# Kernel tuning notes

Hardware: AMD Instinct MI355X
Metric: run time of the kernel (lower is better)

The kernel has to match this reference:

```python
import jax, jax.numpy as jnp
import numpy as np

N = 6144      # total atoms
F = 128       # hidden_dim
NB = 48       # number of molecules (batch segments)
LONG_RANGE_SCALE = 1.0


def setup_inputs() -> dict:
    key = jax.random.key(0)
    ks = jax.random.split(key, 16)
    s = 1.0 / np.sqrt(F)
    return {
        "h0": jax.random.normal(ks[0], (N, F), jnp.float32),
        "h1": jax.random.normal(ks[1], (N, 3, F), jnp.float32),
        "pos": jax.random.normal(ks[2], (N, 3), jnp.float32),
        "batch": jnp.sort(jax.random.randint(ks[3], (N,), 0, NB)),
        "qW1": jax.random.normal(ks[4], (F, F // 2), jnp.float32) * s,
        "qb1": jnp.zeros((F // 2,), jnp.float32),
        "qW2": jax.random.normal(ks[5], (F // 2, 1), jnp.float32) * s,
        "qb2": jnp.zeros((1,), jnp.float32),
        "cW1": jax.random.normal(ks[6], (F, F // 2), jnp.float32) * s,
        "cb1": jnp.zeros((F // 2,), jnp.float32),
        "cW2": jax.random.normal(ks[7], (F // 2, 1), jnp.float32) * s,
        "cb2": jnp.zeros((1,), jnp.float32),
        "muW": jax.random.normal(ks[8], (F, 1), jnp.float32) * s,
    }


def reference(h0, h1, pos, batch, qW1, qb1, qW2, qb2, cW1, cb1, cW2, cb2, muW):
    n = pos.shape[0]
    # pairwise geometry
    batch_mask = batch[:, None] == batch[None, :]                 # (N,N) bool
    diff = pos[:, None, :] - pos[None, :, :]                      # (N,N,3)
    dist_sq = jnp.sum(diff * diff, axis=-1)                       # (N,N)
    dist = jnp.sqrt(dist_sq + 1e-8)
    valid = batch_mask & ~jnp.eye(n, dtype=bool)
    validf = valid.astype(dist.dtype)

    energy = jnp.zeros((), dist.dtype)

    # --- Coulomb (use_charge) ---
    q = jax.nn.silu(h0 @ qW1 + qb1) @ qW2 + qb2                   # (N,1)
    q_sum = jax.ops.segment_sum(q, batch, num_segments=NB)        # (NB,1)
    cnt = jax.ops.segment_sum(jnp.ones((n, 1), q.dtype), batch, num_segments=NB)
    q_mean = q_sum / jnp.maximum(cnt, 1.0)                        # scatter_mean
    q = q - q_mean[batch]                                         # per-molecule neutrality
    qq = q @ q.T                                                  # (N,N)
    f_taper = 1.0 - jnp.exp(-0.5 * dist)
    E_coul = jnp.sum(qq / dist * f_taper * validf)
    energy = energy + 0.5 * E_coul * 14.399

    # --- van der Waals (use_vdw) ---
    c6 = jax.nn.softplus(jax.nn.silu(h0 @ cW1 + cb1) @ cW2 + cb2)  # (N,1), >0
    c6_ij = jnp.sqrt(c6 @ c6.T)                                    # (N,N)
    r6 = dist_sq ** 3
    E_vdw = -jnp.sum(c6_ij / (r6 + 20.0) * validf)
    energy = energy + 0.5 * E_vdw

    # --- dipole-dipole (use_dipole) ---
    mu = (h1 @ muW)[..., 0]                                        # (N,3)
    mu_dot_mu = mu @ mu.T                                          # (N,N)
    n_ij = diff / (dist[..., None] + 1e-8)                         # (N,N,3)
    mu_dot_n_i = jnp.einsum("id,ijd->ij", mu, n_ij)
    mu_dot_n_j = jnp.einsum("jd,ijd->ij", mu, n_ij)
    inv_r3 = 1.0 / (dist_sq * dist + 10.0)
    E_dip = jnp.sum((mu_dot_mu - 3.0 * mu_dot_n_i * mu_dot_n_j) * inv_r3 * validf)
    energy = energy + 0.5 * E_dip

    return energy * LONG_RANGE_SCALE
```

## Files before the change

kernel.cpp:

```cpp
#include <hip/hip_runtime.h>
#include <math.h>

#define F 128
#define H 64
#define HH 32
#define AT 64
#define NBMOL 48
#define CAP 256
#define SPLIT 16

__device__ __forceinline__ float silu_f(float x) {
    return x / (1.0f + __expf(-x));
}
__device__ __forceinline__ float softplus_f(float x) {
    return fmaxf(x, 0.0f) + log1pf(__expf(-fabsf(x)));
}
__device__ __forceinline__ float frcp(float x) {
    return __builtin_amdgcn_rcpf(x);
}
__device__ __forceinline__ float dot4(float4 a, float4 b) {
    return fmaf(a.x, b.x, fmaf(a.y, b.y, fmaf(a.z, b.z, a.w * b.w)));
}

__global__ __launch_bounds__(256, 4) void k_atom(
    const float* __restrict__ h0, const float* __restrict__ h1,
    const int* __restrict__ batch,
    const float* __restrict__ qW1, const float* __restrict__ qb1,
    const float* __restrict__ qW2,
    const float* __restrict__ cW1, const float* __restrict__ cb1,
    const float* __restrict__ cW2,
    const float* __restrict__ muW,
    float* __restrict__ part,
    float* __restrict__ mu,
    int* __restrict__ segstart, int* __restrict__ segend,
    float* __restrict__ out, int N, int nmlp, int ndip)
{
    __shared__ float4 sW4[HH * 32];
    __shared__ float4 sX4[AT * 32];
    __shared__ float red[4][AT];

    const int b = blockIdx.x;
    const int tid = threadIdx.x;

    if (b < nmlp) {
        const int tile  = b >> 2;
        const int net   = b & 1;
        const int hhalf = (b >> 1) & 1;
        const float* __restrict__ W1 = net ? cW1 : qW1;
        const float* __restrict__ b1 = net ? cb1 : qb1;
        const float* __restrict__ W2 = net ? cW2 : qW2;

        for (int idx = tid; idx < HH * F; idx += 256) {
            int f = idx >> 5;
            int hh = idx & 31;
            float val = W1[f * H + hhalf * HH + hh];
            int f4 = f >> 2, fi = f & 3;
            ((float*)&sW4[hh * 32 + (f4 ^ ((hh >> 1) & 7))])[fi] = val;
        }
        const float4* __restrict__ h0v = (const float4*)h0;
        for (int idx = tid; idx < AT * 32; idx += 256) {
            int a = idx >> 5, f4 = idx & 31;
            int row = min(tile * AT + a, N - 1);
            sX4[a * 32 + (f4 ^ ((a >> 2) & 7))] = h0v[(size_t)row * 32 + f4];
        }
        __syncthreads();

        const int ag = tid & 15;
        const int hg = tid >> 4;
        const int swx = ag & 7;
        const int sww = hg & 7;
        const int h0i = hhalf * HH + 2 * hg;

        float z[4][2];
        {
            float b0 = b1[h0i], b1v = b1[h0i + 1];
            #pragma unroll
            for (int j = 0; j < 4; ++j) { z[j][0] = b0; z[j][1] = b1v; }
        }

        #pragma unroll 4
        for (int f4 = 0; f4 < 32; ++f4) {
            float4 w0 = sW4[(2 * hg) * 32 + (f4 ^ sww)];
            float4 w1 = sW4[(2 * hg + 1) * 32 + (f4 ^ sww)];
            #pragma unroll
            for (int j = 0; j < 4; ++j) {
                float4 x = sX4[(4 * ag + j) * 32 + (f4 ^ swx)];
                z[j][0] += dot4(x, w0);
                z[j][1] += dot4(x, w1);
            }
        }

        const float w2a = W2[h0i], w2b = W2[h0i + 1];
        float p[4];
        #pragma unroll
        for (int j = 0; j < 4; ++j)
            p[j] = fmaf(silu_f(z[j][0]), w2a, silu_f(z[j][1]) * w2b);

        #pragma unroll
        for (int j = 0; j < 4; ++j) {
            p[j] += __shfl_xor(p[j], 16);
            p[j] += __shfl_xor(p[j], 32);
        }
        const int wv = tid >> 6, lane = tid & 63;
        if (lane < 16) {
            #pragma unroll
            for (int j = 0; j < 4; ++j) red[wv][4 * lane + j] = p[j];
        }
        __syncthreads();
        if (tid < AT) {
            float s = red[0][tid] + red[1][tid] + red[2][tid] + red[3][tid];
            int atom = tile * AT + tid;
            if (atom < N) part[(size_t)(net * 2 + hhalf) * N + atom] = s;
        }
    } else if (b < nmlp + ndip) {
        const int slot = tid >> 4;
        const int l = tid & 15;
        int row = (b - nmlp) * 16 + slot;
        if (row < 3 * N) {
            const float4* rp = (const float4*)(h1 + (size_t)row * F);
            const float4* mp = (const float4*)muW;
            float pm = dot4(rp[2 * l], mp[2 * l]) +
                       dot4(rp[2 * l + 1], mp[2 * l + 1]);
            #pragma unroll
            for (int off = 1; off < 16; off <<= 1) pm += __shfl_xor(pm, off);
            if (l == 0) mu[row] = pm;
        }
    } else {
        if (tid == 0) out[0] = 0.0f;
        for (int i = tid; i < N; i += 256) {
            int bb = batch[i];
            if (i == 0 || batch[i - 1] != bb) segstart[bb] = i;
            if (i == N - 1 || batch[i + 1] != bb) segend[bb] = i + 1;
        }
    }
}

__global__ __launch_bounds__(256) void k_pair(
    const float* __restrict__ pos,
    const float* __restrict__ part,
    const float* __restrict__ mu,
    const float* __restrict__ qb2, const float* __restrict__ cb2,
    const int* __restrict__ segstart, const int* __restrict__ segend,
    float* __restrict__ out, int N)
{
    const int b = blockIdx.x;
    const int s = blockIdx.y;
    const int tid = threadIdx.x;
    const int st = segstart[b];
    const int n = segend[b] - st;

    const float* __restrict__ p0 = part;
    const float* __restrict__ p1 = part + N;
    const float* __restrict__ p2 = part + 2 * (size_t)N;
    const float* __restrict__ p3 = part + 3 * (size_t)N;
    const float qb2v = qb2[0], cb2v = cb2[0];

    __shared__ float sq[CAP], sc[CAP], sp[3 * CAP], sm[3 * CAP];
    __shared__ float red[4];

    float e_c = 0.f, e_v = 0.f, e_d = 0.f;

    if (n > 1 && n <= CAP) {
        float partsum = 0.f;
        for (int k = tid; k < n; k += 256) {
            float qv = p0[st + k] + p1[st + k] + qb2v;
            sq[k] = qv; partsum += qv;
            sc[k] = sqrtf(softplus_f(p2[st + k] + p3[st + k] + cb2v));
        }
        for (int k = tid; k < 3 * n; k += 256) {
            sp[k] = pos[3 * st + k];
            sm[k] = mu[3 * st + k];
        }
        #pragma unroll
        for (int off = 32; off > 0; off >>= 1)
            partsum += __shfl_xor(partsum, off);
        if ((tid & 63) == 0) red[tid >> 6] = partsum;
        __syncthreads();
        const float mean = (red[0] + red[1] + red[2] + red[3]) / (float)n;

        const int r = tid >> 4;
        const int c = tid & 15;
        for (int il = s + SPLIT * r; il < n; il += SPLIT * 16) {
            const float qi = sq[il] - mean;
            const float sci = sc[il];
            const float xi = sp[3 * il], yi = sp[3 * il + 1], zi = sp[3 * il + 2];
            const float mxi = sm[3 * il], myi = sm[3 * il + 1], mzi = sm[3 * il + 2];
            for (int jl = c; jl < n; jl += 16) {
                if (jl == il) continue;
                float dx = xi - sp[3 * jl], dy = yi - sp[3 * jl + 1],
                      dz = zi - sp[3 * jl + 2];
                float ds0 = fmaf(dx, dx, fmaf(dy, dy, dz * dz));
                float d = sqrtf(ds0 + 1e-8f);
                float inv_d = frcp(d);
                float qj = sq[jl] - mean;
                e_c = fmaf(qi * qj * inv_d, 1.0f - __expf(-0.5f * d), e_c);
                float r6 = ds0 * ds0 * ds0;
                e_v = fmaf(sci * sc[jl], frcp(r6 + 20.0f), e_v);
                float smx = sm[3 * jl], smy = sm[3 * jl + 1], smz = sm[3 * jl + 2];
                float mdm = fmaf(mxi, smx, fmaf(myi, smy, mzi * smz));
                float mdni = fmaf(mxi, dx, fmaf(myi, dy, mzi * dz)) * inv_d;
                float mdnj = fmaf(smx, dx, fmaf(smy, dy, smz * dz)) * inv_d;
                e_d = fmaf(mdm - 3.0f * mdni * mdnj,
                           frcp(fmaf(ds0, d, 10.0f)), e_d);
            }
        }
    } else if (n > CAP) {
        float partsum = 0.f;
        for (int k = tid; k < n; k += 256)
            partsum += p0[st + k] + p1[st + k] + qb2v;
        #pragma unroll
        for (int off = 32; off > 0; off >>= 1)
            partsum += __shfl_xor(partsum, off);
        if ((tid & 63) == 0) red[tid >> 6] = partsum;
        __syncthreads();
        const float mean = (red[0] + red[1] + red[2] + red[3]) / (float)n;
        const int r = tid >> 4, c = tid & 15;
        for (int j0 = 0; j0 < n; j0 += CAP) {
            const int chunk = min(CAP, n - j0);
            __syncthreads();
            for (int k = tid; k < chunk; k += 256) {
                int j = st + j0 + k;
                sq[k] = p0[j] + p1[j] + qb2v;
                sc[k] = sqrtf(softplus_f(p2[j] + p3[j] + cb2v));
            }
            for (int k = tid; k < 3 * chunk; k += 256) {
                sp[k] = pos[3 * (st + j0) + k];
                sm[k] = mu[3 * (st + j0) + k];
            }
            __syncthreads();
            for (int il = s + SPLIT * r; il < n; il += SPLIT * 16) {
                const int i = st + il;
                const float qi = p0[i] + p1[i] + qb2v - mean;
                const float sci = sqrtf(softplus_f(p2[i] + p3[i] + cb2v));
                const float xi = pos[i * 3], yi = pos[i * 3 + 1], zi = pos[i * 3 + 2];
                const float mxi = mu[i * 3], myi = mu[i * 3 + 1], mzi = mu[i * 3 + 2];
                for (int jl = c; jl < chunk; jl += 16) {
                    if (j0 + jl == il) continue;
                    float dx = xi - sp[3 * jl], dy = yi - sp[3 * jl + 1],
                          dz = zi - sp[3 * jl + 2];
                    float ds0 = fmaf(dx, dx, fmaf(dy, dy, dz * dz));
                    float d = sqrtf(ds0 + 1e-8f);
                    float inv_d = frcp(d);
                    float qj = sq[jl] - mean;
                    e_c = fmaf(qi * qj * inv_d, 1.0f - __expf(-0.5f * d), e_c);
                    float r6 = ds0 * ds0 * ds0;
                    e_v = fmaf(sci * sc[jl], frcp(r6 + 20.0f), e_v);
                    float smx = sm[3 * jl], smy = sm[3 * jl + 1], smz = sm[3 * jl + 2];
                    float mdm = fmaf(mxi, smx, fmaf(myi, smy, mzi * smz));
                    float mdni = fmaf(mxi, dx, fmaf(myi, dy, mzi * dz)) * inv_d;
                    float mdnj = fmaf(smx, dx, fmaf(smy, dy, smz * dz)) * inv_d;
                    e_d = fmaf(mdm - 3.0f * mdni * mdnj,
                               frcp(fmaf(ds0, d, 10.0f)), e_d);
                }
            }
        }
    }

    float vv = fmaf(7.1995f, e_c, fmaf(-0.5f, e_v, 0.5f * e_d));
    #pragma unroll
    for (int off = 32; off > 0; off >>= 1) vv += __shfl_xor(vv, off);
    __syncthreads();
    if ((tid & 63) == 0) red[tid >> 6] = vv;
    __syncthreads();
    if (tid == 0) atomicAdd(out, red[0] + red[1] + red[2] + red[3]);
}

extern "C" void kernel_launch(void* const* d_in, const int* in_sizes, int n_in,
                              void* d_out, int out_size, void* d_ws, size_t ws_size,
                              hipStream_t stream) {
    const float* h0  = (const float*)d_in[0];
    const float* h1  = (const float*)d_in[1];
    const float* pos = (const float*)d_in[2];
    const int*   batch = (const int*)d_in[3];
    const float* qW1 = (const float*)d_in[4];
    const float* qb1 = (const float*)d_in[5];
    const float* qW2 = (const float*)d_in[6];
    const float* qb2 = (const float*)d_in[7];
    const float* cW1 = (const float*)d_in[8];
    const float* cb1 = (const float*)d_in[9];
    const float* cW2 = (const float*)d_in[10];
    const float* cb2 = (const float*)d_in[11];
    const float* muW = (const float*)d_in[12];
    float* out = (float*)d_out;
    const int N = in_sizes[0] / F;

    float* ws = (float*)d_ws;
    int* segstart = (int*)ws;
    int* segend   = (int*)(ws + 48);
    float* part = ws + 128;
    float* mu   = part + 4 * (size_t)N;

    const int ntile = (N + AT - 1) / AT;
    const int nmlp = 4 * ntile;
    const int ndip = (3 * N + 15) / 16;
    const int grid = nmlp + ndip + 1;

    k_atom<<<grid, 256, 0, stream>>>(h0, h1, batch, qW1, qb1, qW2,
                                     cW1, cb1, cW2, muW,
                                     part, mu, segstart, segend, out,
                                     N, nmlp, ndip);
    k_pair<<<dim3(NBMOL, SPLIT), 256, 0, stream>>>(pos, part, mu, qb2, cb2,
                                                   segstart, segend, out, N);
}
```

Measured before the change: 113.9 us.

## Split fused atom kernel into MLP and dipole kernels, compute segments in pair kernel

```diff
diff --git a/kernel.cpp b/kernel.cpp
--- a/kernel.cpp
+++ b/kernel.cpp
@@ -22,18 +22,14 @@
     return fmaf(a.x, b.x, fmaf(a.y, b.y, fmaf(a.z, b.z, a.w * b.w)));
 }
 
-__global__ __launch_bounds__(256, 4) void k_atom(
-    const float* __restrict__ h0, const float* __restrict__ h1,
-    const int* __restrict__ batch,
+__global__ __launch_bounds__(256, 3) void k_mlp(
+    const float* __restrict__ h0,
     const float* __restrict__ qW1, const float* __restrict__ qb1,
     const float* __restrict__ qW2,
     const float* __restrict__ cW1, const float* __restrict__ cb1,
     const float* __restrict__ cW2,
-    const float* __restrict__ muW,
     float* __restrict__ part,
-    float* __restrict__ mu,
-    int* __restrict__ segstart, int* __restrict__ segend,
-    float* __restrict__ out, int N, int nmlp, int ndip)
+    float* __restrict__ out, int N)
 {
     __shared__ float4 sW4[HH * 32];
     __shared__ float4 sX4[AT * 32];
@@ -41,122 +37,131 @@
 
     const int b = blockIdx.x;
     const int tid = threadIdx.x;
-
-    if (b < nmlp) {
-        const int tile  = b >> 2;
-        const int net   = b & 1;
-        const int hhalf = (b >> 1) & 1;
-        const float* __restrict__ W1 = net ? cW1 : qW1;
-        const float* __restrict__ b1 = net ? cb1 : qb1;
-        const float* __restrict__ W2 = net ? cW2 : qW2;
-
-        for (int idx = tid; idx < HH * F; idx += 256) {
-            int f = idx >> 5;
-            int hh = idx & 31;
-            float val = W1[f * H + hhalf * HH + hh];
-            int f4 = f >> 2, fi = f & 3;
-            ((float*)&sW4[hh * 32 + (f4 ^ ((hh >> 1) & 7))])[fi] = val;
-        }
-        const float4* __restrict__ h0v = (const float4*)h0;
-        for (int idx = tid; idx < AT * 32; idx += 256) {
-            int a = idx >> 5, f4 = idx & 31;
-            int row = min(tile * AT + a, N - 1);
-            sX4[a * 32 + (f4 ^ ((a >> 2) & 7))] = h0v[(size_t)row * 32 + f4];
-        }
-        __syncthreads();
-
-        const int ag = tid & 15;
-        const int hg = tid >> 4;
-        const int swx = ag & 7;
-        const int sww = hg & 7;
-        const int h0i = hhalf * HH + 2 * hg;
-
-        float z[4][2];
-        {
-            float b0 = b1[h0i], b1v = b1[h0i + 1];
-            #pragma unroll
-            for (int j = 0; j < 4; ++j) { z[j][0] = b0; z[j][1] = b1v; }
-        }
-
-        #pragma unroll 4
-        for (int f4 = 0; f4 < 32; ++f4) {
-            float4 w0 = sW4[(2 * hg) * 32 + (f4 ^ sww)];
-            float4 w1 = sW4[(2 * hg + 1) * 32 + (f4 ^ sww)];
-            #pragma unroll
-            for (int j = 0; j < 4; ++j) {
-                float4 x = sX4[(4 * ag + j) * 32 + (f4 ^ swx)];
-                z[j][0] += dot4(x, w0);
-                z[j][1] += dot4(x, w1);
-            }
-        }
-
-        const float w2a = W2[h0i], w2b = W2[h0i + 1];
-        float p[4];
-        #pragma unroll
-        for (int j = 0; j < 4; ++j)
-            p[j] = fmaf(silu_f(z[j][0]), w2a, silu_f(z[j][1]) * w2b);
-
+    if (b == 0 && tid == 0) out[0] = 0.0f;
+
+    const int tile  = b >> 2;
+    const int net   = b & 1;
+    const int hhalf = (b >> 1) & 1;
+    const float* __restrict__ W1 = net ? cW1 : qW1;
+    const float* __restrict__ b1 = net ? cb1 : qb1;
+    const float* __restrict__ W2 = net ? cW2 : qW2;
+
+    for (int idx = tid; idx < HH * F; idx += 256) {
+        int f = idx >> 5;
+        int hh = idx & 31;
+        float val = W1[f * H + hhalf * HH + hh];
+        int f4 = f >> 2, fi = f & 3;
+        ((float*)&sW4[hh * 32 + (f4 ^ ((hh >> 1) & 7))])[fi] = val;
+    }
+    const float4* __restrict__ h0v = (const float4*)h0;
+    for (int idx = tid; idx < AT * 32; idx += 256) {
+        int a = idx >> 5, f4 = idx & 31;
+        int row = min(tile * AT + a, N - 1);
+        sX4[a * 32 + (f4 ^ ((a >> 2) & 7))] = h0v[(size_t)row * 32 + f4];
+    }
+    __syncthreads();
+
+    const int ag = tid & 15;
+    const int hg = tid >> 4;
+    const int swx = ag & 7;
+    const int sww = hg & 7;
+    const int h0i = hhalf * HH + 2 * hg;
+
+    float z[4][2];
+    {
+        float b0 = b1[h0i], b1v = b1[h0i + 1];
+        #pragma unroll
+        for (int j = 0; j < 4; ++j) { z[j][0] = b0; z[j][1] = b1v; }
+    }
+
+    #pragma unroll 4
+    for (int f4 = 0; f4 < 32; ++f4) {
+        float4 w0 = sW4[(2 * hg) * 32 + (f4 ^ sww)];
+        float4 w1 = sW4[(2 * hg + 1) * 32 + (f4 ^ sww)];
         #pragma unroll
         for (int j = 0; j < 4; ++j) {
-            p[j] += __shfl_xor(p[j], 16);
-            p[j] += __shfl_xor(p[j], 32);
-        }
-        const int wv = tid >> 6, lane = tid & 63;
-        if (lane < 16) {
-            #pragma unroll
-            for (int j = 0; j < 4; ++j) red[wv][4 * lane + j] = p[j];
-        }
-        __syncthreads();
-        if (tid < AT) {
-            float s = red[0][tid] + red[1][tid] + red[2][tid] + red[3][tid];
-            int atom = tile * AT + tid;
-            if (atom < N) part[(size_t)(net * 2 + hhalf) * N + atom] = s;
-        }
-    } else if (b < nmlp + ndip) {
-        const int slot = tid >> 4;
-        const int l = tid & 15;
-        int row = (b - nmlp) * 16 + slot;
-        if (row < 3 * N) {
-            const float4* rp = (const float4*)(h1 + (size_t)row * F);
-            const float4* mp = (const float4*)muW;
-            float pm = dot4(rp[2 * l], mp[2 * l]) +
-                       dot4(rp[2 * l + 1], mp[2 * l + 1]);
-            #pragma unroll
-            for (int off = 1; off < 16; off <<= 1) pm += __shfl_xor(pm, off);
-            if (l == 0) mu[row] = pm;
-        }
-    } else {
-        if (tid == 0) out[0] = 0.0f;
-        for (int i = tid; i < N; i += 256) {
-            int bb = batch[i];
-            if (i == 0 || batch[i - 1] != bb) segstart[bb] = i;
-            if (i == N - 1 || batch[i + 1] != bb) segend[bb] = i + 1;
-        }
+            float4 x = sX4[(4 * ag + j) * 32 + (f4 ^ swx)];
+            z[j][0] += dot4(x, w0);
+            z[j][1] += dot4(x, w1);
+        }
+    }
+
+    const float w2a = W2[h0i], w2b = W2[h0i + 1];
+    float p[4];
+    #pragma unroll
+    for (int j = 0; j < 4; ++j)
+        p[j] = fmaf(silu_f(z[j][0]), w2a, silu_f(z[j][1]) * w2b);
+
+    #pragma unroll
+    for (int j = 0; j < 4; ++j) {
+        p[j] += __shfl_xor(p[j], 16);
+        p[j] += __shfl_xor(p[j], 32);
+    }
+    const int wv = tid >> 6, lane = tid & 63;
+    if (lane < 16) {
+        #pragma unroll
+        for (int j = 0; j < 4; ++j) red[wv][4 * lane + j] = p[j];
+    }
+    __syncthreads();
+    if (tid < AT) {
+        float s = red[0][tid] + red[1][tid] + red[2][tid] + red[3][tid];
+        int atom = tile * AT + tid;
+        if (atom < N) part[(size_t)(net * 2 + hhalf) * N + atom] = s;
+    }
+}
+
+__global__ __launch_bounds__(256, 8) void k_dip(
+    const float* __restrict__ h1, const float* __restrict__ muW,
+    float* __restrict__ mu, int nrows)
+{
+    const int slot = threadIdx.x >> 4;
+    const int l = threadIdx.x & 15;
+    int row = blockIdx.x * 16 + slot;
+    if (row < nrows) {
+        const float4* rp = (const float4*)(h1 + (size_t)row * F);
+        const float4* mp = (const float4*)muW;
+        float pm = dot4(rp[2 * l], mp[2 * l]) +
+                   dot4(rp[2 * l + 1], mp[2 * l + 1]);
+        #pragma unroll
+        for (int off = 1; off < 16; off <<= 1) pm += __shfl_xor(pm, off);
+        if (l == 0) mu[row] = pm;
     }
 }
 
 __global__ __launch_bounds__(256) void k_pair(
     const float* __restrict__ pos,
+    const int* __restrict__ batch,
     const float* __restrict__ part,
     const float* __restrict__ mu,
     const float* __restrict__ qb2, const float* __restrict__ cb2,
-    const int* __restrict__ segstart, const int* __restrict__ segend,
     float* __restrict__ out, int N)
 {
     const int b = blockIdx.x;
     const int s = blockIdx.y;
     const int tid = threadIdx.x;
-    const int st = segstart[b];
-    const int n = segend[b] - st;
+
+    __shared__ int sst, sen;
+    __shared__ float sq[CAP], sc[CAP], sp[3 * CAP], sm[3 * CAP];
+    __shared__ float red[4];
+
+    if (tid == 0) { sst = 0; sen = 0; }
+    __syncthreads();
+    for (int k = tid; k < N; k += 256) {
+        int bk = batch[k];
+        if (bk == b) {
+            if (k == 0 || batch[k - 1] != b) sst = k;
+            if (k == N - 1 || batch[k + 1] != b) sen = k + 1;
+        }
+    }
+    __syncthreads();
+    const int st = sst;
+    const int n = sen - sst;
 
     const float* __restrict__ p0 = part;
     const float* __restrict__ p1 = part + N;
     const float* __restrict__ p2 = part + 2 * (size_t)N;
     const float* __restrict__ p3 = part + 3 * (size_t)N;
     const float qb2v = qb2[0], cb2v = cb2[0];
-
-    __shared__ float sq[CAP], sc[CAP], sp[3 * CAP], sm[3 * CAP];
-    __shared__ float red[4];
 
     float e_c = 0.f, e_v = 0.f, e_d = 0.f;
 
@@ -285,20 +290,15 @@
     const int N = in_sizes[0] / F;
 
     float* ws = (float*)d_ws;
-    int* segstart = (int*)ws;
-    int* segend   = (int*)(ws + 48);
-    float* part = ws + 128;
+    float* part = ws;
     float* mu   = part + 4 * (size_t)N;
 
     const int ntile = (N + AT - 1) / AT;
-    const int nmlp = 4 * ntile;
-    const int ndip = (3 * N + 15) / 16;
-    const int grid = nmlp + ndip + 1;
-
-    k_atom<<<grid, 256, 0, stream>>>(h0, h1, batch, qW1, qb1, qW2,
-                                     cW1, cb1, cW2, muW,
-                                     part, mu, segstart, segend, out,
-                                     N, nmlp, ndip);
-    k_pair<<<dim3(NBMOL, SPLIT), 256, 0, stream>>>(pos, part, mu, qb2, cb2,
-                                                   segstart, segend, out, N);
-}
+    const int nrows = 3 * N;
+
+    k_mlp<<<4 * ntile, 256, 0, stream>>>(h0, qW1, qb1, qW2, cW1, cb1, cW2,
+                                         part, out, N);
+    k_dip<<<(nrows + 15) / 16, 256, 0, stream>>>(h1, muW, mu, nrows);
+    k_pair<<<dim3(NBMOL, SPLIT), 256, 0, stream>>>(pos, batch, part, mu,
+                                                   qb2, cb2, out, N);
+}
```

After: 116.6 us. 2.3% more time.
